# Kernel tuning notes

Hardware: AMD Instinct MI355X
Metric: run time of the kernel (lower is better)

## Reference

```python
import jax, jax.numpy as jnp
import numpy as np

B, T, C = 4, 2048, 1024
QH = 4            # n_q_heads
D = C // QH       # per-head dim = 256
EPS = 1e-5


def setup_inputs() -> dict:
    key = jax.random.key(0)
    k1, k2, k3 = jax.random.split(key, 3)
    residual = jax.random.normal(k1, (B, T, C), dtype=jnp.float32)
    # scale weights ~ Xavier-ish so relu(score)^2 stays numerically sane
    w_fc = jax.random.normal(k2, (C, C), dtype=jnp.float32) * (1.0 / np.sqrt(C))
    w_proj = jax.random.normal(k3, (C, C), dtype=jnp.float32) * (1.0 / np.sqrt(C))
    ln_g = jnp.ones((C,), dtype=jnp.float32)
    ln_b = jnp.zeros((C,), dtype=jnp.float32)
    return {"residual": residual, "w_fc": w_fc, "w_proj": w_proj,
            "ln_g": ln_g, "ln_b": ln_b}


def _layernorm(x, g, b):
    mu = jnp.mean(x, axis=-1, keepdims=True)
    var = jnp.mean(jnp.square(x - mu), axis=-1, keepdims=True)
    return (x - mu) * jax.lax.rsqrt(var + EPS) * g + b


def reference(residual, w_fc, w_proj, ln_g, ln_b):
    Bx, Tx, Cx = residual.shape
    x = _layernorm(residual, ln_g, ln_b)
    # q: (B, QH, T, D)
    q = x.reshape(Bx, Tx, QH, D).transpose(0, 2, 1, 3)
    # keys: rows of w_fc chopped into 4C kv entries of dim D, shared across heads
    k = w_fc.reshape(-1, D)          # (S, D), S = 4C
    # values: columns of w_proj (i.e. w_proj^T rows) chopped the same way
    v = w_proj.T.reshape(-1, D)      # (S, D)
    scores = jnp.einsum('bhtd,sd->bhts', q, k)
    # softmax(log(relusq(score))) then *exp(lse) == plain relu(score)^2 weights
    p = jnp.square(jax.nn.relu(scores))
    out = jnp.einsum('bhts,sd->bhtd', p, v)
    out = out.transpose(0, 2, 1, 3).reshape(Bx, Tx, Cx)
    return residual + out
```

## Files before the change

### kernel.cpp

```cpp
#include <hip/hip_runtime.h>
#include <hip/hip_bf16.h>

typedef __attribute__((ext_vector_type(8))) short bf16x8;
typedef __attribute__((ext_vector_type(4))) float f32x4;
typedef unsigned short ushort_t;

#define C_    1024
#define MROWS 32768
#define D_    256
#define S_TOT 4096
#define SCH   32
#define NCH   (S_TOT / SCH)

__device__ __forceinline__ unsigned short f2bf(float f) {
  union { float f; unsigned int u; } v; v.f = f;
  unsigned int u = v.u;
  u += 0x7fffu + ((u >> 16) & 1u);
  return (unsigned short)(u >> 16);
}

__device__ __forceinline__ void async16(const void* g, void* l) {
  __builtin_amdgcn_global_load_lds(
      (const __attribute__((address_space(1))) unsigned int*)g,
      (__attribute__((address_space(3))) unsigned int*)l, 16, 0, 0);
}

__global__ __launch_bounds__(256) void ln_kernel(const float* __restrict__ res,
                                                 const float* __restrict__ g,
                                                 const float* __restrict__ b,
                                                 unsigned short* __restrict__ xq) {
  int row = blockIdx.x;
  int tid = threadIdx.x;
  const float* r = res + (size_t)row * C_;
  float4 x = *(const float4*)(r + tid * 4);
  float s  = x.x + x.y + x.z + x.w;
  float s2 = x.x * x.x + x.y * x.y + x.z * x.z + x.w * x.w;
  #pragma unroll
  for (int off = 32; off > 0; off >>= 1) {
    s  += __shfl_down(s, off, 64);
    s2 += __shfl_down(s2, off, 64);
  }
  __shared__ float ws[4], ws2[4];
  int wave = tid >> 6, lane = tid & 63;
  if (lane == 0) { ws[wave] = s; ws2[wave] = s2; }
  __syncthreads();
  float ts  = ws[0] + ws[1] + ws[2] + ws[3];
  float ts2 = ws2[0] + ws2[1] + ws2[2] + ws2[3];
  float mu  = ts * (1.0f / C_);
  float var = ts2 * (1.0f / C_) - mu * mu;
  float rs  = rsqrtf(var + 1e-5f);
  int c = tid * 4;
  float4 gg = *(const float4*)(g + c);
  float4 bb = *(const float4*)(b + c);
  unsigned short o[4];
  o[0] = f2bf((x.x - mu) * rs * gg.x + bb.x);
  o[1] = f2bf((x.y - mu) * rs * gg.y + bb.y);
  o[2] = f2bf((x.z - mu) * rs * gg.z + bb.z);
  o[3] = f2bf((x.w - mu) * rs * gg.w + bb.w);
  *(ushort4*)(xq + (size_t)row * C_ + c) = *(ushort4*)o;
}

__global__ __launch_bounds__(256) void prep_k(const float* __restrict__ wfc,
                                              unsigned short* __restrict__ kq) {
  int t = blockIdx.x * 256 + threadIdx.x;
  int lane = t & 63;
  int sn  = (t >> 6) & 1;
  int kc  = (t >> 7) & 7;
  int sc2 = t >> 10;
  int s = sc2 * 32 + sn * 16 + (lane & 15);
  int d = kc * 32 + (lane >> 4) * 8;
  const float* src = wfc + (size_t)s * D_ + d;
  float4 a = *(const float4*)src;
  float4 b = *(const float4*)(src + 4);
  unsigned short o[8] = { f2bf(a.x), f2bf(a.y), f2bf(a.z), f2bf(a.w),
                          f2bf(b.x), f2bf(b.y), f2bf(b.z), f2bf(b.w) };
  *(uint4*)(kq + (size_t)t * 8) = *(uint4*)o;
}

__global__ __launch_bounds__(256) void prep_v(const float* __restrict__ wproj,
                                              unsigned short* __restrict__ vq) {
  __shared__ unsigned short tile[8192];
  int b = blockIdx.x;
  int tid = threadIdx.x;
  int c0 = b * 8;
  #pragma unroll
  for (int it = 0; it < 4; ++it) {
    int row = it * 256 + tid;
    const float* src = wproj + (size_t)row * C_ + c0;
    float4 a = *(const float4*)src;
    float4 bb = *(const float4*)(src + 4);
    unsigned short* dst = &tile[row * 8];
    dst[0] = f2bf(a.x);  dst[1] = f2bf(a.y);  dst[2] = f2bf(a.z);  dst[3] = f2bf(a.w);
    dst[4] = f2bf(bb.x); dst[5] = f2bf(bb.y); dst[6] = f2bf(bb.z); dst[7] = f2bf(bb.w);
  }
  __syncthreads();
  #pragma unroll
  for (int it = 0; it < 4; ++it) {
    int slot = it * 256 + tid;
    int lane = slot & 63;
    int dn   = slot >> 6;
    int d = dn * 16 + (lane & 15);
    int sl0 = (lane >> 4) * 8;
    unsigned short o[8];
    #pragma unroll
    for (int j = 0; j < 8; ++j) {
      int sl = sl0 + j;
      o[j] = tile[((sl & 3) * 256 + d) * 8 + (sl >> 2)];
    }
    *(uint4*)(vq + (size_t)b * 8192 + (size_t)slot * 8) = *(uint4*)o;
  }
}

__global__ __launch_bounds__(256, 1) void mlpmha_main(
    const unsigned short* __restrict__ xq,
    const unsigned short* __restrict__ kq,
    const unsigned short* __restrict__ vq,
    const float* __restrict__ res,
    float* __restrict__ out) {
  __shared__ unsigned short ldsK[2][8192];
  __shared__ unsigned short ldsV[8192];
  __shared__ unsigned short ldsP[128][36];

  int tid  = threadIdx.x;
  int wave = tid >> 6;
  int lane = tid & 63;
  int l16  = lane & 15;
  int quad = lane >> 4;
  int wgM  = blockIdx.x * 128;
  int wrow = wgM + wave * 32;

  bf16x8 qf[2][8];
  #pragma unroll
  for (int mt = 0; mt < 2; ++mt) {
    const unsigned short* qr = xq + (size_t)(wrow + mt * 16 + l16) * D_ + quad * 8;
    #pragma unroll
    for (int kc = 0; kc < 8; ++kc) qf[mt][kc] = *(const bf16x8*)(qr + kc * 32);
  }

  f32x4 acc[8][4];
  #pragma unroll
  for (int i = 0; i < 8; ++i)
    #pragma unroll
    for (int j = 0; j < 4; ++j) acc[i][j] = (f32x4){0.f, 0.f, 0.f, 0.f};

  int soff = wave * 2048 + lane * 8;

  {
    const unsigned short* kg = kq + soff;
    #pragma unroll
    for (int i = 0; i < 4; ++i)
      async16(kg + i * 512, &ldsK[0][soff + i * 512]);
  }
  __syncthreads();

  for (int sc = 0; sc < NCH; ++sc) {
    int cur = sc & 1;

    {
      const unsigned short* vg = vq + (size_t)sc * 8192 + soff;
      #pragma unroll
      for (int i = 0; i < 4; ++i)
        async16(vg + i * 512, &ldsV[soff + i * 512]);
    }

    f32x4 sacc[2][2];
    #pragma unroll
    for (int mt = 0; mt < 2; ++mt)
      #pragma unroll
      for (int sn = 0; sn < 2; ++sn) sacc[mt][sn] = (f32x4){0.f, 0.f, 0.f, 0.f};
    #pragma unroll
    for (int kc = 0; kc < 8; ++kc) {
      #pragma unroll
      for (int sn = 0; sn < 2; ++sn) {
        bf16x8 kb = *(const bf16x8*)&ldsK[cur][(kc * 2 + sn) * 512 + lane * 8];
        #pragma unroll
        for (int mt = 0; mt < 2; ++mt)
          sacc[mt][sn] = __builtin_amdgcn_mfma_f32_16x16x32_bf16(qf[mt][kc], kb, sacc[mt][sn], 0, 0, 0);
      }
    }

    #pragma unroll
    for (int mt = 0; mt < 2; ++mt)
      #pragma unroll
      for (int sn = 0; sn < 2; ++sn)
        #pragma unroll
        for (int r = 0; r < 4; ++r) {
          float v = sacc[mt][sn][r];
          v = v > 0.f ? v * v : 0.f;
          ldsP[wave * 32 + mt * 16 + quad * 4 + r][sn * 16 + l16] = f2bf(v);
        }

    __syncthreads();

    if (sc + 1 < NCH) {
      const unsigned short* kg = kq + (size_t)(sc + 1) * 8192 + soff;
      #pragma unroll
      for (int i = 0; i < 4; ++i)
        async16(kg + i * 512, &ldsK[1 - cur][soff + i * 512]);
    }

    {
      bf16x8 vb[4];
      #pragma unroll
      for (int dnl = 0; dnl < 4; ++dnl)
        vb[dnl] = *(const bf16x8*)&ldsV[((wave * 4 + dnl) * 64 + lane) * 8];
      #pragma unroll
      for (int mt = 0; mt < 8; ++mt) {
        const unsigned short* pp = &ldsP[mt * 16 + l16][quad * 8];
        union { ushort4 h[2]; bf16x8 v; } pu;
        pu.h[0] = *(const ushort4*)pp;
        pu.h[1] = *(const ushort4*)(pp + 4);
        bf16x8 pa = pu.v;
        #pragma unroll
        for (int dnl = 0; dnl < 4; ++dnl)
          acc[mt][dnl] = __builtin_amdgcn_mfma_f32_16x16x32_bf16(pa, vb[dnl], acc[mt][dnl], 0, 0, 0);
      }
    }

    __syncthreads();
  }

  #pragma unroll
  for (int mt = 0; mt < 8; ++mt)
    #pragma unroll
    for (int r = 0; r < 4; ++r) {
      size_t row = (size_t)(wgM + mt * 16 + quad * 4 + r) * D_;
      #pragma unroll
      for (int dnl = 0; dnl < 4; ++dnl) {
        size_t idx = row + wave * 64 + dnl * 16 + l16;
        out[idx] = res[idx] + acc[mt][dnl][r];
      }
    }
}

extern "C" void kernel_launch(void* const* d_in, const int* in_sizes, int n_in,
                              void* d_out, int out_size, void* d_ws, size_t ws_size,
                              hipStream_t stream) {
  const float* res   = (const float*)d_in[0];
  const float* wfc   = (const float*)d_in[1];
  const float* wproj = (const float*)d_in[2];
  const float* g     = (const float*)d_in[3];
  const float* b     = (const float*)d_in[4];
  float* out = (float*)d_out;

  unsigned short* xq = (unsigned short*)d_ws;
  unsigned short* kq = xq + (size_t)MROWS * D_;
  unsigned short* vq = kq + (size_t)S_TOT * D_;

  ln_kernel<<<8192, 256, 0, stream>>>(res, g, b, xq);
  prep_k<<<512, 256, 0, stream>>>(wfc, kq);
  prep_v<<<128, 256, 0, stream>>>(wproj, vq);
  mlpmha_main<<<256, 256, 0, stream>>>(xq, kq, vq, res, out);
}
```

Measured before the change: 299.4 us.

## Split main kernel work across 8 waves and make layernorm one-row-per-wave

The main attention kernel moves from 4 to 8 waves per block. The score phase is split across M and S halves, and the PV phase across M halves and D quarters, which halves the per-wave accumulator registers and the number of async LDS loads per thread. The goal is more latency hiding and better MFMA issue with the same 256-block grid. Separately, layernorm now handles one row per wave using xor shuffles, removing the shared-memory reduction and block barrier. The trade-off is more waves contending at each __syncthreads and a possible change in register pressure under launch_bounds(512,2).

```diff
diff --git a/kernel.cpp b/kernel.cpp
--- a/kernel.cpp
+++ b/kernel.cpp
@@ -3,7 +3,6 @@
 
 typedef __attribute__((ext_vector_type(8))) short bf16x8;
 typedef __attribute__((ext_vector_type(4))) float f32x4;
-typedef unsigned short ushort_t;
 
 #define C_    1024
 #define MROWS 32768
@@ -29,35 +28,37 @@
                                                  const float* __restrict__ g,
                                                  const float* __restrict__ b,
                                                  unsigned short* __restrict__ xq) {
-  int row = blockIdx.x;
-  int tid = threadIdx.x;
+  int wave = threadIdx.x >> 6, lane = threadIdx.x & 63;
+  int row = blockIdx.x * 4 + wave;
   const float* r = res + (size_t)row * C_;
-  float4 x = *(const float4*)(r + tid * 4);
-  float s  = x.x + x.y + x.z + x.w;
-  float s2 = x.x * x.x + x.y * x.y + x.z * x.z + x.w * x.w;
+  float4 x[4];
+  float s = 0.f, s2 = 0.f;
+  #pragma unroll
+  for (int i = 0; i < 4; ++i) {
+    x[i] = *(const float4*)(r + i * 256 + lane * 4);
+    s  += x[i].x + x[i].y + x[i].z + x[i].w;
+    s2 += x[i].x * x[i].x + x[i].y * x[i].y + x[i].z * x[i].z + x[i].w * x[i].w;
+  }
   #pragma unroll
   for (int off = 32; off > 0; off >>= 1) {
-    s  += __shfl_down(s, off, 64);
-    s2 += __shfl_down(s2, off, 64);
-  }
-  __shared__ float ws[4], ws2[4];
-  int wave = tid >> 6, lane = tid & 63;
-  if (lane == 0) { ws[wave] = s; ws2[wave] = s2; }
-  __syncthreads();
-  float ts  = ws[0] + ws[1] + ws[2] + ws[3];
-  float ts2 = ws2[0] + ws2[1] + ws2[2] + ws2[3];
-  float mu  = ts * (1.0f / C_);
-  float var = ts2 * (1.0f / C_) - mu * mu;
+    s  += __shfl_xor(s, off, 64);
+    s2 += __shfl_xor(s2, off, 64);
+  }
+  float mu  = s * (1.0f / C_);
+  float var = s2 * (1.0f / C_) - mu * mu;
   float rs  = rsqrtf(var + 1e-5f);
-  int c = tid * 4;
-  float4 gg = *(const float4*)(g + c);
-  float4 bb = *(const float4*)(b + c);
-  unsigned short o[4];
-  o[0] = f2bf((x.x - mu) * rs * gg.x + bb.x);
-  o[1] = f2bf((x.y - mu) * rs * gg.y + bb.y);
-  o[2] = f2bf((x.z - mu) * rs * gg.z + bb.z);
-  o[3] = f2bf((x.w - mu) * rs * gg.w + bb.w);
-  *(ushort4*)(xq + (size_t)row * C_ + c) = *(ushort4*)o;
+  #pragma unroll
+  for (int i = 0; i < 4; ++i) {
+    int c = i * 256 + lane * 4;
+    float4 gg = *(const float4*)(g + c);
+    float4 bb = *(const float4*)(b + c);
+    unsigned short o[4];
+    o[0] = f2bf((x[i].x - mu) * rs * gg.x + bb.x);
+    o[1] = f2bf((x[i].y - mu) * rs * gg.y + bb.y);
+    o[2] = f2bf((x[i].z - mu) * rs * gg.z + bb.z);
+    o[3] = f2bf((x[i].w - mu) * rs * gg.w + bb.w);
+    *(ushort4*)(xq + (size_t)row * C_ + c) = *(ushort4*)o;
+  }
 }
 
 __global__ __launch_bounds__(256) void prep_k(const float* __restrict__ wfc,
@@ -111,7 +112,7 @@
   }
 }
 
-__global__ __launch_bounds__(256, 1) void mlpmha_main(
+__global__ __launch_bounds__(512, 2) void mlpmha_main(
     const unsigned short* __restrict__ xq,
     const unsigned short* __restrict__ kq,
     const unsigned short* __restrict__ vq,
@@ -127,29 +128,31 @@
   int l16  = lane & 15;
   int quad = lane >> 4;
   int wgM  = blockIdx.x * 128;
-  int wrow = wgM + wave * 32;
+
+  int mi = wave & 3, si = wave >> 2;
+  int ni = wave & 3, mi2 = wave >> 2;
 
   bf16x8 qf[2][8];
   #pragma unroll
   for (int mt = 0; mt < 2; ++mt) {
-    const unsigned short* qr = xq + (size_t)(wrow + mt * 16 + l16) * D_ + quad * 8;
+    const unsigned short* qr =
+        xq + (size_t)(wgM + mi * 32 + mt * 16 + l16) * D_ + quad * 8;
     #pragma unroll
     for (int kc = 0; kc < 8; ++kc) qf[mt][kc] = *(const bf16x8*)(qr + kc * 32);
   }
 
-  f32x4 acc[8][4];
-  #pragma unroll
-  for (int i = 0; i < 8; ++i)
+  f32x4 acc[4][4];
+  #pragma unroll
+  for (int i = 0; i < 4; ++i)
     #pragma unroll
     for (int j = 0; j < 4; ++j) acc[i][j] = (f32x4){0.f, 0.f, 0.f, 0.f};
 
-  int soff = wave * 2048 + lane * 8;
+  int soff = tid * 8;
 
   {
     const unsigned short* kg = kq + soff;
-    #pragma unroll
-    for (int i = 0; i < 4; ++i)
-      async16(kg + i * 512, &ldsK[0][soff + i * 512]);
+    async16(kg, &ldsK[0][soff]);
+    async16(kg + 4096, &ldsK[0][soff + 4096]);
   }
   __syncthreads();
 
@@ -158,62 +161,53 @@
 
     {
       const unsigned short* vg = vq + (size_t)sc * 8192 + soff;
-      #pragma unroll
-      for (int i = 0; i < 4; ++i)
-        async16(vg + i * 512, &ldsV[soff + i * 512]);
-    }
-
-    f32x4 sacc[2][2];
+      async16(vg, &ldsV[soff]);
+      async16(vg + 4096, &ldsV[soff + 4096]);
+    }
+
+    f32x4 sacc[2];
+    sacc[0] = (f32x4){0.f, 0.f, 0.f, 0.f};
+    sacc[1] = (f32x4){0.f, 0.f, 0.f, 0.f};
+    #pragma unroll
+    for (int kc = 0; kc < 8; ++kc) {
+      bf16x8 kb = *(const bf16x8*)&ldsK[cur][(kc * 2 + si) * 512 + lane * 8];
+      #pragma unroll
+      for (int mt = 0; mt < 2; ++mt)
+        sacc[mt] = __builtin_amdgcn_mfma_f32_16x16x32_bf16(qf[mt][kc], kb, sacc[mt], 0, 0, 0);
+    }
+
     #pragma unroll
     for (int mt = 0; mt < 2; ++mt)
       #pragma unroll
-      for (int sn = 0; sn < 2; ++sn) sacc[mt][sn] = (f32x4){0.f, 0.f, 0.f, 0.f};
-    #pragma unroll
-    for (int kc = 0; kc < 8; ++kc) {
-      #pragma unroll
-      for (int sn = 0; sn < 2; ++sn) {
-        bf16x8 kb = *(const bf16x8*)&ldsK[cur][(kc * 2 + sn) * 512 + lane * 8];
-        #pragma unroll
-        for (int mt = 0; mt < 2; ++mt)
-          sacc[mt][sn] = __builtin_amdgcn_mfma_f32_16x16x32_bf16(qf[mt][kc], kb, sacc[mt][sn], 0, 0, 0);
+      for (int r = 0; r < 4; ++r) {
+        float v = sacc[mt][r];
+        v = v > 0.f ? v * v : 0.f;
+        ldsP[mi * 32 + mt * 16 + quad * 4 + r][si * 16 + l16] = f2bf(v);
       }
-    }
-
-    #pragma unroll
-    for (int mt = 0; mt < 2; ++mt)
-      #pragma unroll
-      for (int sn = 0; sn < 2; ++sn)
-        #pragma unroll
-        for (int r = 0; r < 4; ++r) {
-          float v = sacc[mt][sn][r];
-          v = v > 0.f ? v * v : 0.f;
-          ldsP[wave * 32 + mt * 16 + quad * 4 + r][sn * 16 + l16] = f2bf(v);
-        }
 
     __syncthreads();
 
     if (sc + 1 < NCH) {
       const unsigned short* kg = kq + (size_t)(sc + 1) * 8192 + soff;
-      #pragma unroll
-      for (int i = 0; i < 4; ++i)
-        async16(kg + i * 512, &ldsK[1 - cur][soff + i * 512]);
+      async16(kg, &ldsK[1 - cur][soff]);
+      async16(kg + 4096, &ldsK[1 - cur][soff + 4096]);
     }
 
     {
       bf16x8 vb[4];
       #pragma unroll
       for (int dnl = 0; dnl < 4; ++dnl)
-        vb[dnl] = *(const bf16x8*)&ldsV[((wave * 4 + dnl) * 64 + lane) * 8];
-      #pragma unroll
-      for (int mt = 0; mt < 8; ++mt) {
-        const unsigned short* pp = &ldsP[mt * 16 + l16][quad * 8];
+        vb[dnl] = *(const bf16x8*)&ldsV[((ni * 4 + dnl) * 64 + lane) * 8];
+      #pragma unroll
+      for (int mt2 = 0; mt2 < 4; ++mt2) {
+        const unsigned short* pp = &ldsP[mi2 * 64 + mt2 * 16 + l16][quad * 8];
         union { ushort4 h[2]; bf16x8 v; } pu;
         pu.h[0] = *(const ushort4*)pp;
         pu.h[1] = *(const ushort4*)(pp + 4);
         bf16x8 pa = pu.v;
         #pragma unroll
         for (int dnl = 0; dnl < 4; ++dnl)
-          acc[mt][dnl] = __builtin_amdgcn_mfma_f32_16x16x32_bf16(pa, vb[dnl], acc[mt][dnl], 0, 0, 0);
+          acc[mt2][dnl] = __builtin_amdgcn_mfma_f32_16x16x32_bf16(pa, vb[dnl], acc[mt2][dnl], 0, 0, 0);
       }
     }
 
@@ -221,14 +215,14 @@
   }
 
   #pragma unroll
-  for (int mt = 0; mt < 8; ++mt)
+  for (int mt2 = 0; mt2 < 4; ++mt2)
     #pragma unroll
     for (int r = 0; r < 4; ++r) {
-      size_t row = (size_t)(wgM + mt * 16 + quad * 4 + r) * D_;
+      size_t row = (size_t)(wgM + mi2 * 64 + mt2 * 16 + quad * 4 + r) * D_;
       #pragma unroll
       for (int dnl = 0; dnl < 4; ++dnl) {
-        size_t idx = row + wave * 64 + dnl * 16 + l16;
-        out[idx] = res[idx] + acc[mt][dnl][r];
+        size_t idx = row + ni * 64 + dnl * 16 + l16;
+        out[idx] = res[idx] + acc[mt2][dnl][r];
       }
     }
 }
@@ -247,8 +241,8 @@
   unsigned short* kq = xq + (size_t)MROWS * D_;
   unsigned short* vq = kq + (size_t)S_TOT * D_;
 
-  ln_kernel<<<8192, 256, 0, stream>>>(res, g, b, xq);
+  ln_kernel<<<2048, 256, 0, stream>>>(res, g, b, xq);
   prep_k<<<512, 256, 0, stream>>>(wfc, kq);
   prep_v<<<128, 256, 0, stream>>>(wproj, vq);
-  mlpmha_main<<<256, 256, 0, stream>>>(xq, kq, vq, res, out);
-}
+  mlpmha_main<<<256, 512, 0, stream>>>(xq, kq, vq, res, out);
+}
```

Measured after the change: 242.7 us. 18.9% less time.
